# Performance work log

Measured on AMD Instinct MI355X. Metric: run time of the kernel, lower is better.

## Reference

```python
import jax, jax.numpy as jnp
import numpy as np
import math

VOCAB, HID, SEQ, BATCH = 32000, 512, 2048, 32


def setup_inputs() -> dict:
    key = jax.random.key(0)
    ks = jax.random.split(key, 12)
    s = 1.0 / math.sqrt(HID)
    def u(k, shape):
        return jax.random.uniform(k, shape, jnp.float32, -s, s)
    tokens = jax.random.randint(ks[0], (SEQ, BATCH), 0, VOCAB, dtype=jnp.int64)
    return {
        "tokens": tokens,
        "h0": jnp.zeros((BATCH, HID), jnp.float32),
        "embedding": u(ks[1], (VOCAB, HID)),
        "wx_f": u(ks[2], (HID, 4 * HID)), "bx_f": u(ks[3], (4 * HID,)),
        "wh_f": u(ks[4], (HID, 4 * HID)), "bh_f": u(ks[5], (4 * HID,)),
        "wx_b": u(ks[6], (HID, 4 * HID)), "bx_b": u(ks[7], (4 * HID,)),
        "wh_b": u(ks[8], (HID, 4 * HID)), "bh_b": u(ks[9], (4 * HID,)),
    }


def _lstm_scan(emb, h0, wx, bx, wh, bh):
    # emb: [S, B, H]; returns all hidden states [S, B, H]
    def step(carry, x):
        h, c = carry
        gates = x @ wx + bx + h @ wh + bh            # [B, 4H]
        i, f, g, o = jnp.split(gates, 4, axis=-1)     # torch.chunk order
        i = jax.nn.sigmoid(i)
        f = jax.nn.sigmoid(f)
        o = jax.nn.sigmoid(o)
        g = jnp.tanh(g)
        c2 = f * c + i * g
        h2 = o * jnp.tanh(c2)
        return (h2, c2), h2
    (_, _), hs = jax.lax.scan(step, (h0, h0), emb)
    return hs


def reference(tokens, h0, embedding, wx_f, bx_f, wh_f, bh_f, wx_b, bx_b, wh_b, bh_b):
    emb = embedding[tokens]                                  # [S, B, H]
    hf = _lstm_scan(emb, h0, wx_f, bx_f, wh_f, bh_f)         # [S, B, H]
    hb = _lstm_scan(emb[::-1], h0, wx_b, bx_b, wh_b, bh_b)[::-1]
    out = jnp.concatenate([hf, hb], axis=-1)                 # [S, B, 2H]
    # original cats per-step [B,2H] along dim=1 -> [B, S*2H]
    S, B = out.shape[0], out.shape[1]
    return out.transpose(1, 0, 2).reshape(B, S * 2 * HID)
```

## Files before the change

kernel.cpp:

```cpp
#include <hip/hip_runtime.h>
#include <hip/hip_bf16.h>
#include <stdint.h>
#include <stddef.h>

#define SEQ   2048
#define BATCH 32
#define HID   512
#define G4    2048
#define NSL   64
#define UPS   8
#define RING  8
#define FPAD  32

typedef __bf16 bf16;
typedef bf16  bf16x8 __attribute__((ext_vector_type(8)));
typedef float f32x4  __attribute__((ext_vector_type(4)));

__global__ void k_embed(const int* __restrict__ tokens,
                        const float* __restrict__ h0,
                        const float* __restrict__ table,
                        bf16* __restrict__ embT,
                        bf16* __restrict__ hbuf_f,
                        bf16* __restrict__ hbuf_b)
{
    int wid  = (blockIdx.x * blockDim.x + threadIdx.x) >> 6;
    int lane = threadIdx.x & 63;
    int k = lane * 8;
    if (wid < SEQ * BATCH) {
        int tok = tokens[wid];
        const float* src = table + (size_t)tok * HID;
        float4 a = *(const float4*)(src + k);
        float4 b = *(const float4*)(src + k + 4);
        bf16x8 v;
        v[0]=(bf16)a.x; v[1]=(bf16)a.y; v[2]=(bf16)a.z; v[3]=(bf16)a.w;
        v[4]=(bf16)b.x; v[5]=(bf16)b.y; v[6]=(bf16)b.z; v[7]=(bf16)b.w;
        *(bf16x8*)(embT + (size_t)wid * HID + k) = v;
    } else if (wid < SEQ * BATCH + BATCH) {
        int b = wid - SEQ * BATCH;
        const float* src = h0 + (size_t)b * HID;
        bf16x8 v;
        #pragma unroll
        for (int j = 0; j < 8; j++) v[j] = (bf16)src[k + j];
        *(bf16x8*)(hbuf_f + lane * (BATCH * UPS) + b * UPS) = v;
        *(bf16x8*)(hbuf_b + lane * (BATCH * UPS) + b * UPS) = v;
    }
}

__global__ void k_transpose(const float* s0, const float* s1,
                            const float* s2, const float* s3,
                            bf16* __restrict__ dst)
{
    const float* srcs[4] = {s0, s1, s2, s3};
    const float* src = srcs[blockIdx.y];
    bf16* d = dst + (size_t)blockIdx.y * ((size_t)G4 * HID);
    int c = blockIdx.x * 256 + threadIdx.x;
    for (int k = 0; k < HID; k++)
        d[(size_t)c * HID + k] = (bf16)src[(size_t)k * G4 + c];
}

__global__ __launch_bounds__(256, 1) void k_lstm(
    const bf16* __restrict__ embT,
    const bf16* __restrict__ wxT,
    const bf16* __restrict__ whT,
    const float* __restrict__ bx_f, const float* __restrict__ bh_f,
    const float* __restrict__ bx_b, const float* __restrict__ bh_b,
    const float* __restrict__ h0,
    bf16* __restrict__ hbuf_f, bf16* __restrict__ hbuf_b,
    uint32_t* __restrict__ flags_f, uint32_t* __restrict__ flags_b,
    float* __restrict__ out)
{
    __shared__ __align__(16) char smem[32768 + 4608];
    float* gbuf = (float*)(smem + 32768);

    const int tid   = threadIdx.x;
    const int bid   = blockIdx.x;
    const int dir   = bid & 1;
    const int slice = bid >> 1;
    const int u0    = slice * UPS;

    const bf16* wxTs = wxT + (size_t)dir * ((size_t)G4 * HID);
    const bf16* whTs = whT + (size_t)dir * ((size_t)G4 * HID);
    const float* bx  = dir ? bx_b : bx_f;
    const float* bh  = dir ? bh_b : bh_f;
    bf16* hbuf       = dir ? hbuf_b : hbuf_f;
    uint32_t* flags  = dir ? flags_b : flags_f;

    #pragma unroll
    for (int i = 0; i < 8; i++) {
        int e  = i * 2048 + tid * 8;
        int lc = e >> 9;
        int k  = e & 511;
        int c  = (lc >> 3) * HID + u0 + (lc & 7);
        bf16x8 v = *(const bf16x8*)(whTs + (size_t)c * HID + k);
        *(bf16x8*)(smem + lc * 1024 + ((k * 2) ^ ((lc & 7) << 4))) = v;
    }

    const int w     = tid >> 6;
    const int lane  = tid & 63;
    const int mtile = w >> 1;
    const int ntile = w & 1;
    const int lrow  = lane & 15;
    const int lq    = lane >> 4;
    const int lc_b  = ntile * 16 + lrow;
    const int gcol  = (lc_b >> 3) * HID + u0 + (lc_b & 7);
    const float bias = bx[gcol] + bh[gcol];

    const int arow   = mtile * 16 + lrow;
    const int brow_off = lc_b * 1024;
    const int bswz     = (lc_b & 7) << 4;

    const int pb = lane >> 1;
    const int pu = (lane & 1) * 4;
    f32x4 creg = {0.f, 0.f, 0.f, 0.f};
    if (tid < 64)
        creg = *(const f32x4*)(h0 + (size_t)pb * HID + u0 + pu);

    __syncthreads();

    for (int t = 0; t < SEQ; t++) {
        const int s = dir ? (SEQ - 1 - t) : t;

        f32x4 acc = {bias, bias, bias, bias};
        const bf16* aX = embT + ((size_t)s * BATCH + arow) * HID + (lq * 8);
        const bf16* bX = wxTs + (size_t)gcol * HID + (lq * 8);
        #pragma unroll
        for (int kk = 0; kk < 16; kk++) {
            bf16x8 a = *(const bf16x8*)(aX + kk * 32);
            bf16x8 b = *(const bf16x8*)(bX + kk * 32);
            acc = __builtin_amdgcn_mfma_f32_16x16x32_bf16(a, b, acc, 0, 0, 0);
        }

        if (w == 1 && t > 0) {
            const uint32_t* fp = flags + lane * FPAD;
            int rounds = 0;
            uint64_t t0c = 0;
            for (;;) {
                uint32_t v = __hip_atomic_load(fp, __ATOMIC_RELAXED,
                                               __HIP_MEMORY_SCOPE_AGENT);
                if (__all(v >= (uint32_t)t)) break;
                if (!(++rounds & 63)) {
                    uint64_t now = __builtin_amdgcn_s_memrealtime();
                    if (!t0c) t0c = now;
                    else if (now - t0c > 2000000ULL) break;
                }
            }
        }
        __atomic_signal_fence(__ATOMIC_ACQUIRE);
        __syncthreads();

        {
            const unsigned long long* hsrc = (const unsigned long long*)
                ((const char*)hbuf + (size_t)(t & (RING - 1)) * (BATCH * HID) * 2);
            unsigned long long hA[32];
            #pragma unroll
            for (int kk = 0; kk < 16; kk++) {
                int idx = (kk * 4 + lq) * 64 + arow * 2;
                hA[kk * 2]     = __hip_atomic_load(hsrc + idx,
                                     __ATOMIC_RELAXED, __HIP_MEMORY_SCOPE_AGENT);
                hA[kk * 2 + 1] = __hip_atomic_load(hsrc + idx + 1,
                                     __ATOMIC_RELAXED, __HIP_MEMORY_SCOPE_AGENT);
            }
            #pragma unroll
            for (int kk = 0; kk < 16; kk++) {
                union { unsigned long long q[2]; bf16x8 v; } ua;
                ua.q[0] = hA[kk * 2];
                ua.q[1] = hA[kk * 2 + 1];
                int kb = kk * 64 + (lq << 4);
                bf16x8 b = *(const bf16x8*)(smem + brow_off + (kb ^ bswz));
                acc = __builtin_amdgcn_mfma_f32_16x16x32_bf16(ua.v, b, acc, 0, 0, 0);
            }
        }

        {
            int r0 = mtile * 16 + lq * 4;
            #pragma unroll
            for (int r = 0; r < 4; r++)
                gbuf[(r0 + r) * 36 + lc_b] = acc[r];
        }
        __syncthreads();

        if (tid < 64) {
            f32x4 gi = *(const f32x4*)(gbuf + pb * 36 + pu);
            f32x4 gf = *(const f32x4*)(gbuf + pb * 36 + 8 + pu);
            f32x4 gg = *(const f32x4*)(gbuf + pb * 36 + 16 + pu);
            f32x4 go = *(const f32x4*)(gbuf + pb * 36 + 24 + pu);
            float hv[4];
            #pragma unroll
            for (int j = 0; j < 4; j++) {
                float si = 1.f / (1.f + __expf(-gi[j]));
                float sf = 1.f / (1.f + __expf(-gf[j]));
                float so = 1.f / (1.f + __expf(-go[j]));
                float e2 = __expf(2.f * gg[j]);
                float tg = (e2 - 1.f) / (e2 + 1.f);
                creg[j] = sf * creg[j] + si * tg;
                float ec = __expf(2.f * creg[j]);
                float tc = (ec - 1.f) / (ec + 1.f);
                hv[j] = so * tc;
            }
            union { bf16 h[4]; unsigned long long q; } pk;
            #pragma unroll
            for (int j = 0; j < 4; j++) pk.h[j] = (bf16)hv[j];
            __hip_atomic_store(
                (unsigned long long*)(hbuf
                    + (size_t)((t + 1) & (RING - 1)) * (BATCH * HID)
                    + slice * (BATCH * UPS) + pb * UPS + pu),
                pk.q, __ATOMIC_RELAXED, __HIP_MEMORY_SCOPE_AGENT);
            __atomic_signal_fence(__ATOMIC_SEQ_CST);
            __builtin_amdgcn_s_waitcnt(0x0F70);
            if (tid == 0)
                __hip_atomic_store(&flags[slice * FPAD], (uint32_t)(t + 1),
                                   __ATOMIC_RELAXED, __HIP_MEMORY_SCOPE_AGENT);
            f32x4 ov = {hv[0], hv[1], hv[2], hv[3]};
            __builtin_nontemporal_store(ov,
                (f32x4*)(out + (size_t)pb * ((size_t)SEQ * 2 * HID)
                         + (size_t)s * (2 * HID) + dir * HID + u0 + pu));
        }
    }
}

extern "C" void kernel_launch(void* const* d_in, const int* in_sizes, int n_in,
                              void* d_out, int out_size, void* d_ws, size_t ws_size,
                              hipStream_t stream)
{
    const int*   tokens = (const int*)  d_in[0];
    const float* h0     = (const float*)d_in[1];
    const float* table  = (const float*)d_in[2];
    const float* wx_f   = (const float*)d_in[3];
    const float* bx_f   = (const float*)d_in[4];
    const float* wh_f   = (const float*)d_in[5];
    const float* bh_f   = (const float*)d_in[6];
    const float* wx_b   = (const float*)d_in[7];
    const float* bx_b   = (const float*)d_in[8];
    const float* wh_b   = (const float*)d_in[9];
    const float* bh_b   = (const float*)d_in[10];
    float* out = (float*)d_out;
    char*  ws  = (char*)d_ws;

    const size_t OFF_EMBT  = 0;
    const size_t OFF_HF    = 67108864ULL;
    const size_t OFF_HB    = OFF_HF  + 262144ULL;
    const size_t OFF_WXT   = OFF_HB  + 262144ULL;
    const size_t OFF_WHT   = OFF_WXT + 4194304ULL;
    const size_t OFF_FLAGS = OFF_WHT + 4194304ULL;

    bf16* embT   = (bf16*)(ws + OFF_EMBT);
    bf16* hbuf_f = (bf16*)(ws + OFF_HF);
    bf16* hbuf_b = (bf16*)(ws + OFF_HB);
    bf16* wxT    = (bf16*)(ws + OFF_WXT);
    bf16* whT    = (bf16*)(ws + OFF_WHT);
    uint32_t* flags_f = (uint32_t*)(ws + OFF_FLAGS);
    uint32_t* flags_b = (uint32_t*)(ws + OFF_FLAGS + 8192);

    (void)hipMemsetAsync(ws + OFF_FLAGS, 0, 16384, stream);

    {
        int waves  = SEQ * BATCH + BATCH;
        int blocks = (waves * 64 + 255) / 256;
        k_embed<<<blocks, 256, 0, stream>>>(tokens, h0, table, embT, hbuf_f, hbuf_b);
    }
    k_transpose<<<dim3(8, 4), 256, 0, stream>>>(wx_f, wx_b, wh_f, wh_b, wxT);

    k_lstm<<<128, 256, 0, stream>>>(embT, wxT, whT,
                                    bx_f, bh_f, bx_b, bh_b, h0,
                                    hbuf_f, hbuf_b, flags_f, flags_b, out);
}
```

Before: 9.432 ms.

## Replace per-slice flag polling with sentinel-tagged hidden-state ring polling

Drops the separate flag array and its store-wait-then-flag handshake. Hidden-state ring slots are now pre-filled with an all-ones bf16 sentinel, and each wave polls its own h loads until no sentinel remains. Producers clear a slot a few steps ahead, and the gate buffer is double-buffered to remove one block barrier per step. This aims to cut the cross-block sync latency on the serial recurrence. In exchange it relies on 0xFFFF never being a real output value and uses a much shorter timeout, which could let a step proceed on stale data.

```diff
diff --git a/kernel.cpp b/kernel.cpp
--- a/kernel.cpp
+++ b/kernel.cpp
@@ -10,7 +10,6 @@
 #define NSL   64
 #define UPS   8
 #define RING  8
-#define FPAD  32
 
 typedef __bf16 bf16;
 typedef bf16  bf16x8 __attribute__((ext_vector_type(8)));
@@ -66,11 +65,11 @@
     const float* __restrict__ bx_b, const float* __restrict__ bh_b,
     const float* __restrict__ h0,
     bf16* __restrict__ hbuf_f, bf16* __restrict__ hbuf_b,
-    uint32_t* __restrict__ flags_f, uint32_t* __restrict__ flags_b,
     float* __restrict__ out)
 {
-    __shared__ __align__(16) char smem[32768 + 4608];
-    float* gbuf = (float*)(smem + 32768);
+    __shared__ __align__(16) char smem[32768 + 2 * 4608];
+    float* gbuf0 = (float*)(smem + 32768);
+    float* gbuf1 = (float*)(smem + 32768 + 4608);
 
     const int tid   = threadIdx.x;
     const int bid   = blockIdx.x;
@@ -83,7 +82,6 @@
     const float* bx  = dir ? bx_b : bx_f;
     const float* bh  = dir ? bh_b : bh_f;
     bf16* hbuf       = dir ? hbuf_b : hbuf_f;
-    uint32_t* flags  = dir ? flags_b : flags_f;
 
     #pragma unroll
     for (int i = 0; i < 8; i++) {
@@ -119,6 +117,19 @@
 
     for (int t = 0; t < SEQ; t++) {
         const int s = dir ? (SEQ - 1 - t) : t;
+        float* gbuf = (t & 1) ? gbuf1 : gbuf0;
+
+        const unsigned long long* hsrc = (const unsigned long long*)
+            ((const char*)hbuf + (size_t)(t & (RING - 1)) * (BATCH * HID) * 2);
+        unsigned long long hA[32];
+        #pragma unroll
+        for (int kk = 0; kk < 16; kk++) {
+            int idx = (kk * 4 + lq) * 64 + arow * 2;
+            hA[kk * 2]     = __hip_atomic_load(hsrc + idx,
+                                 __ATOMIC_RELAXED, __HIP_MEMORY_SCOPE_AGENT);
+            hA[kk * 2 + 1] = __hip_atomic_load(hsrc + idx + 1,
+                                 __ATOMIC_RELAXED, __HIP_MEMORY_SCOPE_AGENT);
+        }
 
         f32x4 acc = {bias, bias, bias, bias};
         const bf16* aX = embT + ((size_t)s * BATCH + arow) * HID + (lq * 8);
@@ -130,45 +141,56 @@
             acc = __builtin_amdgcn_mfma_f32_16x16x32_bf16(a, b, acc, 0, 0, 0);
         }
 
-        if (w == 1 && t > 0) {
-            const uint32_t* fp = flags + lane * FPAD;
+        {
+            unsigned pend = 0xFFFFu;
             int rounds = 0;
             uint64_t t0c = 0;
             for (;;) {
-                uint32_t v = __hip_atomic_load(fp, __ATOMIC_RELAXED,
-                                               __HIP_MEMORY_SCOPE_AGENT);
-                if (__all(v >= (uint32_t)t)) break;
-                if (!(++rounds & 63)) {
+                unsigned np = 0;
+                #pragma unroll
+                for (int kk = 0; kk < 16; kk++) {
+                    if ((pend >> kk) & 1) {
+                        unsigned long long q0 = hA[kk * 2];
+                        unsigned long long q1 = hA[kk * 2 + 1];
+                        bool bad =
+                            (((unsigned)q0 & 0xFFFFu) == 0xFFFFu) ||
+                            (((unsigned)(q0 >> 32) & 0xFFFFu) == 0xFFFFu) ||
+                            (((unsigned)q1 & 0xFFFFu) == 0xFFFFu) ||
+                            (((unsigned)(q1 >> 32) & 0xFFFFu) == 0xFFFFu);
+                        np |= bad ? (1u << kk) : 0u;
+                    }
+                }
+                pend = np;
+                if (__all(pend == 0)) break;
+                if (!(++rounds & 31)) {
                     uint64_t now = __builtin_amdgcn_s_memrealtime();
                     if (!t0c) t0c = now;
-                    else if (now - t0c > 2000000ULL) break;
+                    else if (now - t0c > 10000ULL) break;
+                }
+                __builtin_amdgcn_s_sleep(2);
+                #pragma unroll
+                for (int kk = 0; kk < 16; kk++) {
+                    if ((pend >> kk) & 1) {
+                        int idx = (kk * 4 + lq) * 64 + arow * 2;
+                        hA[kk * 2]     = __hip_atomic_load(hsrc + idx,
+                                             __ATOMIC_RELAXED,
+                                             __HIP_MEMORY_SCOPE_AGENT);
+                        hA[kk * 2 + 1] = __hip_atomic_load(hsrc + idx + 1,
+                                             __ATOMIC_RELAXED,
+                                             __HIP_MEMORY_SCOPE_AGENT);
+                    }
                 }
             }
         }
-        __atomic_signal_fence(__ATOMIC_ACQUIRE);
-        __syncthreads();
-
-        {
-            const unsigned long long* hsrc = (const unsigned long long*)
-                ((const char*)hbuf + (size_t)(t & (RING - 1)) * (BATCH * HID) * 2);
-            unsigned long long hA[32];
-            #pragma unroll
-            for (int kk = 0; kk < 16; kk++) {
-                int idx = (kk * 4 + lq) * 64 + arow * 2;
-                hA[kk * 2]     = __hip_atomic_load(hsrc + idx,
-                                     __ATOMIC_RELAXED, __HIP_MEMORY_SCOPE_AGENT);
-                hA[kk * 2 + 1] = __hip_atomic_load(hsrc + idx + 1,
-                                     __ATOMIC_RELAXED, __HIP_MEMORY_SCOPE_AGENT);
-            }
-            #pragma unroll
-            for (int kk = 0; kk < 16; kk++) {
-                union { unsigned long long q[2]; bf16x8 v; } ua;
-                ua.q[0] = hA[kk * 2];
-                ua.q[1] = hA[kk * 2 + 1];
-                int kb = kk * 64 + (lq << 4);
-                bf16x8 b = *(const bf16x8*)(smem + brow_off + (kb ^ bswz));
-                acc = __builtin_amdgcn_mfma_f32_16x16x32_bf16(ua.v, b, acc, 0, 0, 0);
-            }
+
+        #pragma unroll
+        for (int kk = 0; kk < 16; kk++) {
+            union { unsigned long long q[2]; bf16x8 v; } ua;
+            ua.q[0] = hA[kk * 2];
+            ua.q[1] = hA[kk * 2 + 1];
+            int kb = kk * 64 + (lq << 4);
+            bf16x8 b = *(const bf16x8*)(smem + brow_off + (kb ^ bswz));
+            acc = __builtin_amdgcn_mfma_f32_16x16x32_bf16(ua.v, b, acc, 0, 0, 0);
         }
 
         {
@@ -200,16 +222,16 @@
             union { bf16 h[4]; unsigned long long q; } pk;
             #pragma unroll
             for (int j = 0; j < 4; j++) pk.h[j] = (bf16)hv[j];
+            const size_t myoff = slice * (BATCH * UPS) + pb * UPS + pu;
             __hip_atomic_store(
                 (unsigned long long*)(hbuf
-                    + (size_t)((t + 1) & (RING - 1)) * (BATCH * HID)
-                    + slice * (BATCH * UPS) + pb * UPS + pu),
+                    + (size_t)((t + 1) & (RING - 1)) * (BATCH * HID) + myoff),
                 pk.q, __ATOMIC_RELAXED, __HIP_MEMORY_SCOPE_AGENT);
-            __atomic_signal_fence(__ATOMIC_SEQ_CST);
-            __builtin_amdgcn_s_waitcnt(0x0F70);
-            if (tid == 0)
-                __hip_atomic_store(&flags[slice * FPAD], (uint32_t)(t + 1),
-                                   __ATOMIC_RELAXED, __HIP_MEMORY_SCOPE_AGENT);
+            __hip_atomic_store(
+                (unsigned long long*)(hbuf
+                    + (size_t)((t + 5) & (RING - 1)) * (BATCH * HID) + myoff),
+                0xFFFFFFFFFFFFFFFFULL,
+                __ATOMIC_RELAXED, __HIP_MEMORY_SCOPE_AGENT);
             f32x4 ov = {hv[0], hv[1], hv[2], hv[3]};
             __builtin_nontemporal_store(ov,
                 (f32x4*)(out + (size_t)pb * ((size_t)SEQ * 2 * HID)
@@ -241,17 +263,14 @@
     const size_t OFF_HB    = OFF_HF  + 262144ULL;
     const size_t OFF_WXT   = OFF_HB  + 262144ULL;
     const size_t OFF_WHT   = OFF_WXT + 4194304ULL;
-    const size_t OFF_FLAGS = OFF_WHT + 4194304ULL;
 
     bf16* embT   = (bf16*)(ws + OFF_EMBT);
     bf16* hbuf_f = (bf16*)(ws + OFF_HF);
     bf16* hbuf_b = (bf16*)(ws + OFF_HB);
     bf16* wxT    = (bf16*)(ws + OFF_WXT);
     bf16* whT    = (bf16*)(ws + OFF_WHT);
-    uint32_t* flags_f = (uint32_t*)(ws + OFF_FLAGS);
-    uint32_t* flags_b = (uint32_t*)(ws + OFF_FLAGS + 8192);
-
-    (void)hipMemsetAsync(ws + OFF_FLAGS, 0, 16384, stream);
+
+    (void)hipMemsetAsync(ws + OFF_HF, 0xFF, 2ULL * 262144ULL, stream);
 
     {
         int waves  = SEQ * BATCH + BATCH;
@@ -262,5 +281,5 @@
 
     k_lstm<<<128, 256, 0, stream>>>(embT, wxT, whT,
                                     bx_f, bh_f, bx_b, bh_b, h0,
-                                    hbuf_f, hbuf_b, flags_f, flags_b, out);
-}
+                                    hbuf_f, hbuf_b, out);
+}
```

New measurement: 12.06 ms. 27.9% more time.

## Pin each LSTM direction to one XCD with 16 wider workgroups

Applied to the files above, without the earlier changes.

Launches 256 workgroups and elects, per XCD, up to 16 workgroups to run the recurrence. Each direction is confined to a single XCD chosen by XCD-id parity, so cross-workgroup h exchange and flag polling stay within one XCD's L2 instead of crossing chips. Each workgroup now owns 32 hidden units (128 gate columns, 128KB of Wh in LDS) rather than 8, which cuts the number of participants per barrier from 64 to 16. Sync uses sc0 loads and a plain volatile flag store after __syncthreads. The election and spin timeouts are fragile: if an XCD gets fewer than 16 blocks, or a timeout fires, results would be wrong.

```diff
diff --git a/kernel.cpp b/kernel.cpp
--- a/kernel.cpp
+++ b/kernel.cpp
@@ -7,21 +7,31 @@
 #define BATCH 32
 #define HID   512
 #define G4    2048
-#define NSL   64
-#define UPS   8
+#define NWG   16
+#define UE    32
 #define RING  8
-#define FPAD  32
 
 typedef __bf16 bf16;
-typedef bf16  bf16x8 __attribute__((ext_vector_type(8)));
-typedef float f32x4  __attribute__((ext_vector_type(4)));
+typedef bf16     bf16x8 __attribute__((ext_vector_type(8)));
+typedef float    f32x4  __attribute__((ext_vector_type(4)));
+typedef unsigned u32x4v __attribute__((ext_vector_type(4)));
+
+__device__ __forceinline__ uint32_t ld_sc0_u32(const volatile uint32_t* p) {
+    uint32_t v;
+    asm volatile("global_load_dword %0, %1, off sc0\n\ts_waitcnt vmcnt(0)"
+                 : "=v"(v) : "v"(p) : "memory");
+    return v;
+}
+__device__ __forceinline__ u32x4v ld_sc0_b128(const void* p) {
+    u32x4v v;
+    asm volatile("global_load_dwordx4 %0, %1, off sc0"
+                 : "=v"(v) : "v"(p) : "memory");
+    return v;
+}
 
 __global__ void k_embed(const int* __restrict__ tokens,
-                        const float* __restrict__ h0,
                         const float* __restrict__ table,
-                        bf16* __restrict__ embT,
-                        bf16* __restrict__ hbuf_f,
-                        bf16* __restrict__ hbuf_b)
+                        bf16* __restrict__ embT)
 {
     int wid  = (blockIdx.x * blockDim.x + threadIdx.x) >> 6;
     int lane = threadIdx.x & 63;
@@ -35,14 +45,6 @@
         v[0]=(bf16)a.x; v[1]=(bf16)a.y; v[2]=(bf16)a.z; v[3]=(bf16)a.w;
         v[4]=(bf16)b.x; v[5]=(bf16)b.y; v[6]=(bf16)b.z; v[7]=(bf16)b.w;
         *(bf16x8*)(embT + (size_t)wid * HID + k) = v;
-    } else if (wid < SEQ * BATCH + BATCH) {
-        int b = wid - SEQ * BATCH;
-        const float* src = h0 + (size_t)b * HID;
-        bf16x8 v;
-        #pragma unroll
-        for (int j = 0; j < 8; j++) v[j] = (bf16)src[k + j];
-        *(bf16x8*)(hbuf_f + lane * (BATCH * UPS) + b * UPS) = v;
-        *(bf16x8*)(hbuf_b + lane * (BATCH * UPS) + b * UPS) = v;
     }
 }
 
@@ -66,124 +68,170 @@
     const float* __restrict__ bx_b, const float* __restrict__ bh_b,
     const float* __restrict__ h0,
     bf16* __restrict__ hbuf_f, bf16* __restrict__ hbuf_b,
-    uint32_t* __restrict__ flags_f, uint32_t* __restrict__ flags_b,
+    int* __restrict__ ectl,
+    uint32_t* __restrict__ flags,
     float* __restrict__ out)
 {
-    __shared__ __align__(16) char smem[32768 + 4608];
-    float* gbuf = (float*)(smem + 32768);
-
-    const int tid   = threadIdx.x;
-    const int bid   = blockIdx.x;
-    const int dir   = bid & 1;
-    const int slice = bid >> 1;
-    const int u0    = slice * UPS;
+    __shared__ __align__(16) char smem[131072 + 16896];
+    float* gbuf = (float*)(smem + 131072);
+
+    const int tid = threadIdx.x;
+
+    int xcd;
+    asm volatile("s_getreg_b32 %0, hwreg(HW_REG_XCC_ID)" : "=s"(xcd));
+    __shared__ int sctl[2];
+    if (tid == 0) {
+        int rank = __hip_atomic_fetch_add(&ectl[xcd], 1, __ATOMIC_RELAXED,
+                                          __HIP_MEMORY_SCOPE_AGENT);
+        int par = xcd & 1;
+        if (rank == 0) {
+            int expd = 0;
+            __hip_atomic_compare_exchange_strong(&ectl[8 + par], &expd, xcd + 1,
+                __ATOMIC_RELAXED, __ATOMIC_RELAXED, __HIP_MEMORY_SCOPE_AGENT);
+        }
+        int e = 0;
+        uint64_t t0 = __builtin_amdgcn_s_memrealtime();
+        for (;;) {
+            e = __hip_atomic_load(&ectl[8 + par], __ATOMIC_RELAXED,
+                                  __HIP_MEMORY_SCOPE_AGENT);
+            if (e) break;
+            if (__builtin_amdgcn_s_memrealtime() - t0 > 100000ULL) break;
+            __builtin_amdgcn_s_sleep(8);
+        }
+        sctl[0] = rank; sctl[1] = e;
+    }
+    __syncthreads();
+    const int  rank   = sctl[0];
+    const bool is_eng = (sctl[1] == xcd + 1) && (rank < NWG);
+    if (!is_eng) return;
+    const int dir = xcd & 1;
+    const int g   = rank;
 
     const bf16* wxTs = wxT + (size_t)dir * ((size_t)G4 * HID);
     const bf16* whTs = whT + (size_t)dir * ((size_t)G4 * HID);
     const float* bx  = dir ? bx_b : bx_f;
     const float* bh  = dir ? bh_b : bh_f;
     bf16* hbuf       = dir ? hbuf_b : hbuf_f;
-    uint32_t* flags  = dir ? flags_b : flags_f;
+    volatile uint32_t* myflag = flags + dir * 512 + g * 32;
+    const uint32_t* fbase     = flags + dir * 512;
 
     #pragma unroll
-    for (int i = 0; i < 8; i++) {
+    for (int i = 0; i < 32; i++) {
         int e  = i * 2048 + tid * 8;
         int lc = e >> 9;
         int k  = e & 511;
-        int c  = (lc >> 3) * HID + u0 + (lc & 7);
-        bf16x8 v = *(const bf16x8*)(whTs + (size_t)c * HID + k);
+        int grow = (lc >> 5) * HID + g * UE + (lc & 31);
+        bf16x8 v = *(const bf16x8*)(whTs + (size_t)grow * HID + k);
         *(bf16x8*)(smem + lc * 1024 + ((k * 2) ^ ((lc & 7) << 4))) = v;
     }
 
     const int w     = tid >> 6;
     const int lane  = tid & 63;
     const int mtile = w >> 1;
-    const int ntile = w & 1;
+    const int ng    = w & 1;
     const int lrow  = lane & 15;
     const int lq    = lane >> 4;
-    const int lc_b  = ntile * 16 + lrow;
-    const int gcol  = (lc_b >> 3) * HID + u0 + (lc_b & 7);
-    const float bias = bx[gcol] + bh[gcol];
-
-    const int arow   = mtile * 16 + lrow;
-    const int brow_off = lc_b * 1024;
-    const int bswz     = (lc_b & 7) << 4;
-
-    const int pb = lane >> 1;
-    const int pu = (lane & 1) * 4;
-    f32x4 creg = {0.f, 0.f, 0.f, 0.f};
-    if (tid < 64)
-        creg = *(const f32x4*)(h0 + (size_t)pb * HID + u0 + pu);
-
+    const int arow  = mtile * 16 + lrow;
+
+    float bias_nt[4];
+    const bf16* bXp[4];
+    #pragma unroll
+    for (int nt = 0; nt < 4; nt++) {
+        int lcb  = ng * 64 + nt * 16 + lrow;
+        int gcol = (lcb >> 5) * HID + g * UE + (lcb & 31);
+        bias_nt[nt] = bx[gcol] + bh[gcol];
+        bXp[nt] = wxTs + (size_t)gcol * HID + lq * 8;
+    }
+    const int b0off = (ng * 64 + lrow) * 1024;
+    const int bswz  = (lrow & 7) << 4;
+
+    const int pb = tid >> 3;
+    const int pu = (tid & 7) << 2;
+    const int kbblk = g * 4 + (pu >> 3);
+
+    f32x4 creg = *(const f32x4*)(h0 + (size_t)pb * HID + g * UE + pu);
+    {
+        union { bf16 h[4]; unsigned long long q; } pk;
+        #pragma unroll
+        for (int j = 0; j < 4; j++) pk.h[j] = (bf16)creg[j];
+        *(volatile unsigned long long*)(hbuf + (size_t)(kbblk * 32 + pb) * 8
+                                        + (pu & 7)) = pk.q;
+    }
     __syncthreads();
+    if (tid == 0) *myflag = 1;
 
     for (int t = 0; t < SEQ; t++) {
         const int s = dir ? (SEQ - 1 - t) : t;
 
-        f32x4 acc = {bias, bias, bias, bias};
-        const bf16* aX = embT + ((size_t)s * BATCH + arow) * HID + (lq * 8);
-        const bf16* bX = wxTs + (size_t)gcol * HID + (lq * 8);
+        f32x4 acc[4];
+        #pragma unroll
+        for (int nt = 0; nt < 4; nt++)
+            acc[nt] = f32x4{bias_nt[nt], bias_nt[nt], bias_nt[nt], bias_nt[nt]};
+        const bf16* aXp = embT + ((size_t)s * BATCH + arow) * HID + lq * 8;
         #pragma unroll
         for (int kk = 0; kk < 16; kk++) {
-            bf16x8 a = *(const bf16x8*)(aX + kk * 32);
-            bf16x8 b = *(const bf16x8*)(bX + kk * 32);
-            acc = __builtin_amdgcn_mfma_f32_16x16x32_bf16(a, b, acc, 0, 0, 0);
-        }
-
-        if (w == 1 && t > 0) {
-            const uint32_t* fp = flags + lane * FPAD;
+            bf16x8 a = *(const bf16x8*)(aXp + kk * 32);
+            #pragma unroll
+            for (int nt = 0; nt < 4; nt++) {
+                bf16x8 b = *(const bf16x8*)(bXp[nt] + kk * 32);
+                acc[nt] = __builtin_amdgcn_mfma_f32_16x16x32_bf16(a, b, acc[nt], 0, 0, 0);
+            }
+        }
+
+        {
+            const uint32_t* fp = fbase + (lane & 15) * 32;
             int rounds = 0;
             uint64_t t0c = 0;
             for (;;) {
-                uint32_t v = __hip_atomic_load(fp, __ATOMIC_RELAXED,
-                                               __HIP_MEMORY_SCOPE_AGENT);
-                if (__all(v >= (uint32_t)t)) break;
+                uint32_t v = ld_sc0_u32(fp);
+                if (__all(v >= (uint32_t)(t + 1))) break;
                 if (!(++rounds & 63)) {
                     uint64_t now = __builtin_amdgcn_s_memrealtime();
                     if (!t0c) t0c = now;
-                    else if (now - t0c > 2000000ULL) break;
+                    else if (now - t0c > 10000ULL) break;
                 }
             }
         }
-        __atomic_signal_fence(__ATOMIC_ACQUIRE);
+
+        {
+            const char* hb = (const char*)hbuf + (size_t)(t & (RING - 1)) * 32768
+                             + ((lq * 32 + arow) << 4);
+            u32x4v hA[16];
+            #pragma unroll
+            for (int kk = 0; kk < 16; kk++)
+                hA[kk] = ld_sc0_b128(hb + kk * 2048);
+            asm volatile("s_waitcnt vmcnt(0)" ::: "memory");
+            __builtin_amdgcn_sched_barrier(0);
+            #pragma unroll
+            for (int kk = 0; kk < 16; kk++) {
+                union { u32x4v u; bf16x8 v; } ua;
+                ua.u = hA[kk];
+                const int kb = kk * 64 + (lq << 4);
+                #pragma unroll
+                for (int nt = 0; nt < 4; nt++) {
+                    bf16x8 b = *(const bf16x8*)(smem + b0off + nt * 16384 + (kb ^ bswz));
+                    acc[nt] = __builtin_amdgcn_mfma_f32_16x16x32_bf16(ua.v, b, acc[nt], 0, 0, 0);
+                }
+            }
+        }
+
+        {
+            const int r0 = mtile * 16 + lq * 4;
+            #pragma unroll
+            for (int nt = 0; nt < 4; nt++) {
+                const int lc = ng * 64 + nt * 16 + lrow;
+                #pragma unroll
+                for (int r = 0; r < 4; r++)
+                    gbuf[(r0 + r) * 132 + lc] = acc[nt][r];
+            }
+        }
         __syncthreads();
 
         {
-            const unsigned long long* hsrc = (const unsigned long long*)
-                ((const char*)hbuf + (size_t)(t & (RING - 1)) * (BATCH * HID) * 2);
-            unsigned long long hA[32];
-            #pragma unroll
-            for (int kk = 0; kk < 16; kk++) {
-                int idx = (kk * 4 + lq) * 64 + arow * 2;
-                hA[kk * 2]     = __hip_atomic_load(hsrc + idx,
-                                     __ATOMIC_RELAXED, __HIP_MEMORY_SCOPE_AGENT);
-                hA[kk * 2 + 1] = __hip_atomic_load(hsrc + idx + 1,
-                                     __ATOMIC_RELAXED, __HIP_MEMORY_SCOPE_AGENT);
-            }
-            #pragma unroll
-            for (int kk = 0; kk < 16; kk++) {
-                union { unsigned long long q[2]; bf16x8 v; } ua;
-                ua.q[0] = hA[kk * 2];
-                ua.q[1] = hA[kk * 2 + 1];
-                int kb = kk * 64 + (lq << 4);
-                bf16x8 b = *(const bf16x8*)(smem + brow_off + (kb ^ bswz));
-                acc = __builtin_amdgcn_mfma_f32_16x16x32_bf16(ua.v, b, acc, 0, 0, 0);
-            }
-        }
-
-        {
-            int r0 = mtile * 16 + lq * 4;
-            #pragma unroll
-            for (int r = 0; r < 4; r++)
-                gbuf[(r0 + r) * 36 + lc_b] = acc[r];
-        }
-        __syncthreads();
-
-        if (tid < 64) {
-            f32x4 gi = *(const f32x4*)(gbuf + pb * 36 + pu);
-            f32x4 gf = *(const f32x4*)(gbuf + pb * 36 + 8 + pu);
-            f32x4 gg = *(const f32x4*)(gbuf + pb * 36 + 16 + pu);
-            f32x4 go = *(const f32x4*)(gbuf + pb * 36 + 24 + pu);
+            f32x4 gi = *(const f32x4*)(gbuf + pb * 132 + pu);
+            f32x4 gf = *(const f32x4*)(gbuf + pb * 132 + 32 + pu);
+            f32x4 gg = *(const f32x4*)(gbuf + pb * 132 + 64 + pu);
+            f32x4 go = *(const f32x4*)(gbuf + pb * 132 + 96 + pu);
             float hv[4];
             #pragma unroll
             for (int j = 0; j < 4; j++) {
@@ -200,20 +248,15 @@
             union { bf16 h[4]; unsigned long long q; } pk;
             #pragma unroll
             for (int j = 0; j < 4; j++) pk.h[j] = (bf16)hv[j];
-            __hip_atomic_store(
-                (unsigned long long*)(hbuf
-                    + (size_t)((t + 1) & (RING - 1)) * (BATCH * HID)
-                    + slice * (BATCH * UPS) + pb * UPS + pu),
-                pk.q, __ATOMIC_RELAXED, __HIP_MEMORY_SCOPE_AGENT);
-            __atomic_signal_fence(__ATOMIC_SEQ_CST);
-            __builtin_amdgcn_s_waitcnt(0x0F70);
-            if (tid == 0)
-                __hip_atomic_store(&flags[slice * FPAD], (uint32_t)(t + 1),
-                                   __ATOMIC_RELAXED, __HIP_MEMORY_SCOPE_AGENT);
+            *(volatile unsigned long long*)(hbuf
+                + (size_t)((t + 1) & (RING - 1)) * 16384
+                + (size_t)(kbblk * 32 + pb) * 8 + (pu & 7)) = pk.q;
+            __syncthreads();
+            if (tid == 0) *myflag = (uint32_t)(t + 2);
             f32x4 ov = {hv[0], hv[1], hv[2], hv[3]};
             __builtin_nontemporal_store(ov,
                 (f32x4*)(out + (size_t)pb * ((size_t)SEQ * 2 * HID)
-                         + (size_t)s * (2 * HID) + dir * HID + u0 + pu));
+                         + (size_t)s * (2 * HID) + dir * HID + g * UE + pu));
         }
     }
 }
@@ -241,26 +284,26 @@
     const size_t OFF_HB    = OFF_HF  + 262144ULL;
     const size_t OFF_WXT   = OFF_HB  + 262144ULL;
     const size_t OFF_WHT   = OFF_WXT + 4194304ULL;
-    const size_t OFF_FLAGS = OFF_WHT + 4194304ULL;
+    const size_t OFF_CTL   = OFF_WHT + 4194304ULL;
+    const size_t OFF_FLAGS = OFF_CTL + 128ULL;
 
     bf16* embT   = (bf16*)(ws + OFF_EMBT);
     bf16* hbuf_f = (bf16*)(ws + OFF_HF);
     bf16* hbuf_b = (bf16*)(ws + OFF_HB);
     bf16* wxT    = (bf16*)(ws + OFF_WXT);
     bf16* whT    = (bf16*)(ws + OFF_WHT);
-    uint32_t* flags_f = (uint32_t*)(ws + OFF_FLAGS);
-    uint32_t* flags_b = (uint32_t*)(ws + OFF_FLAGS + 8192);
-
-    (void)hipMemsetAsync(ws + OFF_FLAGS, 0, 16384, stream);
+    int*      ectl  = (int*)(ws + OFF_CTL);
+    uint32_t* flags = (uint32_t*)(ws + OFF_FLAGS);
+
+    (void)hipMemsetAsync(ws + OFF_CTL, 0, 128 + 4096, stream);
 
     {
-        int waves  = SEQ * BATCH + BATCH;
-        int blocks = (waves * 64 + 255) / 256;
-        k_embed<<<blocks, 256, 0, stream>>>(tokens, h0, table, embT, hbuf_f, hbuf_b);
+        int blocks = (SEQ * BATCH * 64) / 256;
+        k_embed<<<blocks, 256, 0, stream>>>(tokens, table, embT);
     }
     k_transpose<<<dim3(8, 4), 256, 0, stream>>>(wx_f, wx_b, wh_f, wh_b, wxT);
 
-    k_lstm<<<128, 256, 0, stream>>>(embT, wxT, whT,
+    k_lstm<<<256, 256, 0, stream>>>(embT, wxT, whT,
                                     bx_f, bh_f, bx_b, bh_b, h0,
-                                    hbuf_f, hbuf_b, flags_f, flags_b, out);
-}
+                                    hbuf_f, hbuf_b, ectl, flags, out);
+}
```

Measured after the change: 15.28 ms. +62.0%, slower.
